# Performance work log

Hardware: AMD Instinct MI355X
Metric: run time of the kernel (lower is better)

The kernel has to match this reference:

```python
import jax, jax.numpy as jnp
import numpy as np
import math

D_MODEL = 1024
N_HEAD = 16
HEAD_DIM = D_MODEL // N_HEAD
SEQ_LEN = 512
INIT_SIZE = 1568  # from RelativeSinusoidalPositionalEmbedding default


def _rel_pos_embedding(seq_len, embedding_dim):
    # Replicates RelativeSinusoidalPositionalEmbedding with init_size=1568
    num_embeddings = INIT_SIZE + 1  # 1569
    half_dim = embedding_dim // 2
    scale = math.log(10000.0) / (half_dim - 1)
    freqs = np.exp(np.arange(half_dim, dtype=np.float32) * -scale)
    pos = np.arange(-(num_embeddings // 2), num_embeddings // 2, dtype=np.float32)  # [-785, 784)
    emb = pos[:, None] * freqs[None, :]
    weights = np.concatenate([np.sin(emb), np.cos(emb)], axis=1).astype(np.float32)  # (1569, d)
    weights[0, :] = 0.0  # padding_idx
    origin_shift = num_embeddings // 2 + 1  # 785
    positions = np.arange(-seq_len, seq_len) + origin_shift
    embed = weights[positions]  # (2*seq_len, d)
    return jnp.asarray(embed.T)  # (d, 2*seq_len), matching .T in __init__


def setup_inputs() -> dict:
    key = jax.random.key(0)
    k1, k2, k3, k4, k5 = jax.random.split(key, 5)
    x = jax.random.normal(k1, (8, SEQ_LEN, D_MODEL), dtype=jnp.float32)
    prev = jax.random.normal(k2, (8, N_HEAD, SEQ_LEN, SEQ_LEN), dtype=jnp.float32)
    # Linear(d_model, 3*d_model, bias=False): store as (d_model, 3*d_model) for x @ W
    Wqkv = jax.random.normal(k3, (D_MODEL, 3 * D_MODEL), dtype=jnp.float32) / math.sqrt(D_MODEL)
    r_r_bias = jax.random.normal(k4, (1, N_HEAD, 1, HEAD_DIM), dtype=jnp.float32) * 0.02
    r_w_bias = jax.random.normal(k5, (1, N_HEAD, 1, HEAD_DIM), dtype=jnp.float32) * 0.02
    rel_pos = _rel_pos_embedding(SEQ_LEN, HEAD_DIM)  # (head_dim, 2*seq_len)
    return {"x": x, "prev": prev, "Wqkv": Wqkv, "r_r_bias": r_r_bias,
            "r_w_bias": r_w_bias, "rel_pos": rel_pos, "skip_op": 1}


def _shift(BD, seq_len):
    # BD: (b, h, L, 2L) -> (b, h, L, L) via Transformer-XL pad/reshape trick
    b, h, L, two_L = BD.shape
    BD = jnp.pad(BD, ((0, 0), (0, 0), (0, 0), (0, 1)))        # (b,h,L,2L+1)
    BD = BD.reshape(b, h, -1, L)                               # (b,h,2L+1,L)
    BD = BD[:, :, :-1].reshape(b, h, L, -1)                    # (b,h,L,2L)
    return BD[:, :, :, seq_len:]                               # (b,h,L,L)


def reference(x, prev, Wqkv, r_r_bias, r_w_bias, rel_pos, skip_op):
    b, L, d = x.shape
    qkv = x @ Wqkv                                             # (b,L,3d)
    q, k, v = jnp.split(qkv, 3, axis=-1)
    q = q.reshape(b, L, N_HEAD, HEAD_DIM).transpose(0, 2, 1, 3)  # (b,h,L,hd)
    k = k.reshape(b, L, N_HEAD, HEAD_DIM).transpose(0, 2, 1, 3)
    v = v.reshape(b, L, N_HEAD, HEAD_DIM).transpose(0, 2, 1, 3)

    AC = jnp.einsum('bhqd,bhkd->bhqk', q + r_r_bias, k)
    BD = jnp.einsum('bhqd,dp->bhqp', q + r_w_bias, rel_pos)    # (b,h,L,2L)
    BD = _shift(BD, SEQ_LEN)
    E = jnp.einsum('bhkd,dp->bhkp', k, rel_pos)
    E = _shift(E, SEQ_LEN).transpose(0, 1, 3, 2)
    attn_score = (AC + BD + E) / math.sqrt(HEAD_DIM)
    if skip_op:
        attn_score = attn_score + prev
    prev_out = attn_score
    attn = jax.nn.softmax(attn_score, axis=-1)
    out = jnp.einsum('bhqk,bhkd->bhqd', attn, v)
    out = out.transpose(0, 2, 1, 3).reshape(b, L, d)
    return out, prev_out
```

## Files before the change

### kernel.cpp

```cpp
#include <hip/hip_runtime.h>
#include <hip/hip_bf16.h>
#include <math.h>

namespace {
constexpr int Bn = 8;
constexpr int Hn = 16;
constexpr int Ln = 512;
constexpr int HD = 64;
constexpr int DM = 1024;
constexpr int TL = 1024;
constexpr size_t QS  = (size_t)Bn * Hn * Ln * HD;
constexpr size_t FSz = (size_t)Hn * Ln * Ln;
constexpr size_t WN  = (size_t)DM * 3 * DM;
}

typedef __bf16 bf16x8 __attribute__((ext_vector_type(8)));
typedef float f32x4 __attribute__((ext_vector_type(4)));

typedef __attribute__((address_space(1))) void as1_void_t;
typedef __attribute__((address_space(3))) void as3_void_t;

__device__ __forceinline__ void gload_lds16(const void* g, void* l) {
  __builtin_amdgcn_global_load_lds((as1_void_t*)g, (as3_void_t*)l, 16, 0, 0);
}

__device__ __forceinline__ unsigned short f2bf(float f) {
  unsigned int u = __float_as_uint(f);
  u += 0x7fffu + ((u >> 16) & 1u);
  return (unsigned short)(u >> 16);
}
__device__ __forceinline__ float bf2f(unsigned short h) {
  return __uint_as_float(((unsigned int)h) << 16);
}

__global__ __launch_bounds__(256) void conv_x(const float* __restrict__ x,
                                              unsigned short* __restrict__ xh,
                                              unsigned short* __restrict__ xl) {
  size_t i = ((size_t)blockIdx.x * 256 + threadIdx.x) * 4;
  float4 v = *(const float4*)(x + i);
  unsigned short h0 = f2bf(v.x), h1 = f2bf(v.y), h2 = f2bf(v.z), h3 = f2bf(v.w);
  ushort4 hv = make_ushort4(h0, h1, h2, h3);
  ushort4 lv = make_ushort4(f2bf(v.x - bf2f(h0)), f2bf(v.y - bf2f(h1)),
                            f2bf(v.z - bf2f(h2)), f2bf(v.w - bf2f(h3)));
  *(ushort4*)(xh + i) = hv;
  *(ushort4*)(xl + i) = lv;
}

__global__ __launch_bounds__(256) void conv_w(const float* __restrict__ W,
                                              unsigned short* __restrict__ wh,
                                              unsigned short* __restrict__ wl) {
  __shared__ unsigned short Th[64][72];
  __shared__ unsigned short Tl[64][72];
  const int t = threadIdx.x;
  const int n0 = blockIdx.x * 64;
  const int k0 = blockIdx.y * 64;
#pragma unroll
  for (int i = 0; i < 4; ++i) {
    int row = i * 16 + (t >> 4);
    int col = (t & 15) * 4;
    float4 v = *(const float4*)(W + (size_t)(k0 + row) * 3072 + n0 + col);
    unsigned short h;
    h = f2bf(v.x); Th[row][col + 0] = h; Tl[row][col + 0] = f2bf(v.x - bf2f(h));
    h = f2bf(v.y); Th[row][col + 1] = h; Tl[row][col + 1] = f2bf(v.y - bf2f(h));
    h = f2bf(v.z); Th[row][col + 2] = h; Tl[row][col + 2] = f2bf(v.z - bf2f(h));
    h = f2bf(v.w); Th[row][col + 3] = h; Tl[row][col + 3] = f2bf(v.w - bf2f(h));
  }
  __syncthreads();
  const int rn = t & 63, qq = t >> 6;
  unsigned int hw[8], lw[8];
#pragma unroll
  for (int j = 0; j < 8; ++j) {
    unsigned short a = Th[qq * 16 + 2 * j][rn], b = Th[qq * 16 + 2 * j + 1][rn];
    hw[j] = (unsigned int)a | ((unsigned int)b << 16);
    unsigned short c = Tl[qq * 16 + 2 * j][rn], d = Tl[qq * 16 + 2 * j + 1][rn];
    lw[j] = (unsigned int)c | ((unsigned int)d << 16);
  }
  size_t o = (size_t)(n0 + rn) * 1024 + k0 + qq * 16;
  *(uint4*)(wh + o)     = make_uint4(hw[0], hw[1], hw[2], hw[3]);
  *(uint4*)(wh + o + 8) = make_uint4(hw[4], hw[5], hw[6], hw[7]);
  *(uint4*)(wl + o)     = make_uint4(lw[0], lw[1], lw[2], lw[3]);
  *(uint4*)(wl + o + 8) = make_uint4(lw[4], lw[5], lw[6], lw[7]);
}

__global__ __launch_bounds__(256, 2) void qkv_mfma(const unsigned short* __restrict__ xh,
                                                   const unsigned short* __restrict__ xl,
                                                   const unsigned short* __restrict__ wh,
                                                   const unsigned short* __restrict__ wl,
                                                   const float* __restrict__ rrb,
                                                   float* __restrict__ qarr,
                                                   float* __restrict__ karr,
                                                   unsigned short* __restrict__ qrh,
                                                   unsigned short* __restrict__ qrl,
                                                   unsigned short* __restrict__ kharr,
                                                   unsigned short* __restrict__ klarr,
                                                   unsigned short* __restrict__ vTh,
                                                   unsigned short* __restrict__ vTl) {
  __shared__ alignas(16) unsigned short Ah[128 * 32];
  __shared__ alignas(16) unsigned short Al[128 * 32];
  __shared__ alignas(16) unsigned short Bh[128 * 32];
  __shared__ alignas(16) unsigned short Bl[128 * 32];
  const int t = threadIdx.x;
  const int lane = t & 63;
  const int w = t >> 6;
  const int m0 = blockIdx.y * 128;
  const int n0 = blockIdx.x * 128;
  const int wr = w >> 1, wc = w & 1;
  const int l16 = lane & 15, s = lane >> 4;

  const unsigned short* gsrc = (w == 0) ? xh : (w == 1) ? xl : (w == 2) ? wh : wl;
  unsigned short* lbase = (w == 0) ? Ah : (w == 1) ? Al : (w == 2) ? Bh : Bl;
  const int rbase = (w < 2) ? m0 : n0;
  const int srow = lane >> 2, sc = lane & 3;

  int aoff[4], boff[4];
#pragma unroll
  for (int f = 0; f < 4; ++f) {
    int Rm = wr * 64 + f * 16 + l16;
    aoff[f] = Rm * 64 + ((s ^ ((Rm >> 1) & 3)) << 4);
    int Rn = wc * 64 + f * 16 + l16;
    boff[f] = Rn * 64 + ((s ^ ((Rn >> 1) & 3)) << 4);
  }

  f32x4 acc[4][4];
#pragma unroll
  for (int i = 0; i < 4; ++i)
#pragma unroll
    for (int j = 0; j < 4; ++j) acc[i][j] = (f32x4){0.f, 0.f, 0.f, 0.f};

  const char* Ahc = (const char*)Ah;
  const char* Alc = (const char*)Al;
  const char* Bhc = (const char*)Bh;
  const char* Blc = (const char*)Bl;

  for (int k0 = 0; k0 < 1024; k0 += 32) {
#pragma unroll
    for (int u = 0; u < 8; ++u) {
      int row = u * 16 + srow;
      int chunk = sc ^ ((row >> 1) & 3);
      gload_lds16(gsrc + (size_t)(rbase + row) * 1024 + k0 + chunk * 8,
                  lbase + u * 512);
    }
    __syncthreads();

    bf16x8 a_h[4], a_l[4], b_h[4], b_l[4];
#pragma unroll
    for (int f = 0; f < 4; ++f) {
      a_h[f] = *(const bf16x8*)(Ahc + aoff[f]);
      b_h[f] = *(const bf16x8*)(Bhc + boff[f]);
    }
#pragma unroll
    for (int i = 0; i < 4; ++i)
#pragma unroll
      for (int j = 0; j < 4; ++j)
        acc[i][j] = __builtin_amdgcn_mfma_f32_16x16x32_bf16(a_h[i], b_h[j], acc[i][j], 0, 0, 0);
#pragma unroll
    for (int f = 0; f < 4; ++f) b_l[f] = *(const bf16x8*)(Blc + boff[f]);
#pragma unroll
    for (int i = 0; i < 4; ++i)
#pragma unroll
      for (int j = 0; j < 4; ++j)
        acc[i][j] = __builtin_amdgcn_mfma_f32_16x16x32_bf16(a_h[i], b_l[j], acc[i][j], 0, 0, 0);
#pragma unroll
    for (int f = 0; f < 4; ++f) a_l[f] = *(const bf16x8*)(Alc + aoff[f]);
#pragma unroll
    for (int i = 0; i < 4; ++i)
#pragma unroll
      for (int j = 0; j < 4; ++j)
        acc[i][j] = __builtin_amdgcn_mfma_f32_16x16x32_bf16(a_l[i], b_h[j], acc[i][j], 0, 0, 0);
    __syncthreads();
  }

  const int part = n0 >> 10;
  const int nb = n0 & 1023;
#pragma unroll
  for (int i = 0; i < 4; ++i) {
#pragma unroll
    for (int j = 0; j < 4; ++j) {
      const int n = nb + wc * 64 + j * 16 + l16;
      const int h = n >> 6, d = n & 63;
      const int mb = m0 + wr * 64 + i * 16 + (lane >> 4) * 4;
      const int bb = mb >> 9, lb = mb & 511;
      const size_t rowbase = ((size_t)(bb * Hn + h) * Ln + lb) << 6;
      if (part == 0) {
        const float rr = rrb[h * HD + d];
#pragma unroll
        for (int r = 0; r < 4; ++r) {
          const float v = acc[i][j][r];
          const size_t qi = rowbase + ((size_t)r << 6) + d;
          qarr[qi] = v;
          const float qv = v + rr;
          const unsigned short hh = f2bf(qv);
          qrh[qi] = hh;
          qrl[qi] = f2bf(qv - bf2f(hh));
        }
      } else if (part == 1) {
#pragma unroll
        for (int r = 0; r < 4; ++r) {
          const float v = acc[i][j][r];
          const size_t qi = rowbase + ((size_t)r << 6) + d;
          karr[qi] = v;
          const unsigned short hh = f2bf(v);
          kharr[qi] = hh;
          klarr[qi] = f2bf(v - bf2f(hh));
        }
      } else {
        ushort4 hv, lv;
        unsigned short* hp = &hv.x;
        unsigned short* lp = &lv.x;
#pragma unroll
        for (int r = 0; r < 4; ++r) {
          const float v = acc[i][j][r];
          const unsigned short hh = f2bf(v);
          hp[r] = hh;
          lp[r] = f2bf(v - bf2f(hh));
        }
        const size_t vi = ((size_t)(bb * Hn + h) * HD + d) * Ln + lb;
        *(ushort4*)(vTh + vi) = hv;
        *(ushort4*)(vTl + vi) = lv;
      }
    }
  }
}

__global__ __launch_bounds__(256) void fg_gemm(const float* __restrict__ qarr,
                                               const float* __restrict__ karr,
                                               const float* __restrict__ rwb,
                                               const float* __restrict__ R,
                                               float* __restrict__ Fs,
                                               float* __restrict__ Gs,
                                               int b) {
  const int m0 = blockIdx.y * 64;
  const int n0 = blockIdx.x * 64;
  if (m0 + n0 + 126 < 512 || m0 + n0 >= 1024) return;

  __shared__ float As[64][68];
  __shared__ float Rs[64][68];
  const int t = threadIdx.x;
  const int h = blockIdx.z >> 1;
  const int which = blockIdx.z & 1;
  const float* A = (which == 0 ? qarr : karr) + (size_t)(b * Hn + h) * Ln * HD;

#pragma unroll
  for (int i = 0; i < 4; ++i) {
    int idx = t + i * 256;
    int r = idx >> 4;
    int c4 = (idx & 15) * 4;
    float4 av = *(const float4*)(A + (size_t)(m0 + r) * HD + c4);
    if (which == 0) {
      float4 bv = *(const float4*)(rwb + h * HD + c4);
      av.x += bv.x; av.y += bv.y; av.z += bv.z; av.w += bv.w;
    }
    As[c4 + 0][r] = av.x; As[c4 + 1][r] = av.y;
    As[c4 + 2][r] = av.z; As[c4 + 3][r] = av.w;
    *(float4*)(&Rs[r][c4]) = *(const float4*)(R + (size_t)r * TL + n0 + c4);
  }
  __syncthreads();
  const int tr = t >> 4, tc = t & 15;
  float acc[4][4];
#pragma unroll
  for (int i = 0; i < 4; ++i)
#pragma unroll
    for (int j = 0; j < 4; ++j) acc[i][j] = 0.f;
#pragma unroll 16
  for (int kk = 0; kk < 64; ++kk) {
    float a[4], bb[4];
    *(float4*)(a)  = *(const float4*)(&As[kk][tr * 4]);
    *(float4*)(bb) = *(const float4*)(&Rs[kk][tc * 4]);
#pragma unroll
    for (int i = 0; i < 4; ++i)
#pragma unroll
      for (int j = 0; j < 4; ++j) acc[i][j] = fmaf(a[i], bb[j], acc[i][j]);
  }
  if (which == 0) {
    float* O = Fs + (size_t)h * Ln * Ln;
#pragma unroll
    for (int i = 0; i < 4; ++i) {
      const int q = m0 + tr * 4 + i;
#pragma unroll
      for (int jj = 0; jj < 4; ++jj) {
        const int p = n0 + tc * 4 + jj;
        const int j = p + q - 512;
        if ((unsigned)j < 512u) O[((size_t)q << 9) + j] = acc[i][jj];
      }
    }
  } else {
    float* O = Gs + (size_t)h * Ln * Ln;
#pragma unroll
    for (int i = 0; i < 4; ++i) {
      const int jrow = m0 + tr * 4 + i;
#pragma unroll
      for (int jj = 0; jj < 4; ++jj) {
        const int p = n0 + tc * 4 + jj;
        const int q = p + jrow - 512;
        if ((unsigned)q < 512u) O[((size_t)q << 9) + jrow] = acc[i][jj];
      }
    }
  }
}

__global__ __launch_bounds__(64) void attn_mfma(const unsigned short* __restrict__ qrh,
                                                const unsigned short* __restrict__ qrl,
                                                const unsigned short* __restrict__ kharr,
                                                const unsigned short* __restrict__ klarr,
                                                const unsigned short* __restrict__ vTh,
                                                const unsigned short* __restrict__ vTl,
                                                const float* __restrict__ Fs,
                                                const float* __restrict__ Gs,
                                                const float* __restrict__ prev,
                                                const int* __restrict__ skip,
                                                float* __restrict__ out,
                                                float* __restrict__ pout,
                                                int b) {
  __shared__ alignas(16) unsigned short PhL[16 * 64];
  __shared__ alignas(16) unsigned short PlL[16 * 64];
  const int lane = threadIdx.x & 63;
  const int s = lane >> 4, l16 = lane & 15;
  const int h = blockIdx.y;
  const int q0 = blockIdx.x * 16;
  const size_t bh = (size_t)(b * Hn + h);
  const float pf = (skip[0] != 0) ? 1.f : 0.f;

  bf16x8 aqh[2], aql[2];
#pragma unroll
  for (int kd = 0; kd < 2; ++kd) {
    const size_t a = ((bh * Ln + q0 + l16) << 6) + kd * 32 + s * 8;
    aqh[kd] = *(const bf16x8*)(qrh + a);
    aql[kd] = *(const bf16x8*)(qrl + a);
  }

  float m_run[4] = {-INFINITY, -INFINITY, -INFINITY, -INFINITY};
  float l_run[4] = {0.f, 0.f, 0.f, 0.f};
  f32x4 O[4];
#pragma unroll
  for (int fo = 0; fo < 4; ++fo) O[fo] = (f32x4){0.f, 0.f, 0.f, 0.f};

  const int qrow = q0 + s * 4;

  for (int jt = 0; jt < 8; ++jt) {
    const int j0 = jt * 64;

    f32x4 S[4];
#pragma unroll
    for (int fi = 0; fi < 4; ++fi) S[fi] = (f32x4){0.f, 0.f, 0.f, 0.f};
#pragma unroll
    for (int kd = 0; kd < 2; ++kd) {
#pragma unroll
      for (int fi = 0; fi < 4; ++fi) {
        const size_t ka = ((bh * Ln + j0 + fi * 16 + l16) << 6) + kd * 32 + s * 8;
        const bf16x8 bkh = *(const bf16x8*)(kharr + ka);
        const bf16x8 bkl = *(const bf16x8*)(klarr + ka);
        S[fi] = __builtin_amdgcn_mfma_f32_16x16x32_bf16(aqh[kd], bkh, S[fi], 0, 0, 0);
        S[fi] = __builtin_amdgcn_mfma_f32_16x16x32_bf16(aqh[kd], bkl, S[fi], 0, 0, 0);
        S[fi] = __builtin_amdgcn_mfma_f32_16x16x32_bf16(aql[kd], bkh, S[fi], 0, 0, 0);
      }
    }

    float sc[4][4];
    float mx[4] = {-INFINITY, -INFINITY, -INFINITY, -INFINITY};
#pragma unroll
    for (int fi = 0; fi < 4; ++fi) {
      const int j = j0 + fi * 16 + l16;
#pragma unroll
      for (int r = 0; r < 4; ++r) {
        const int q = qrow + r;
        const size_t fb = (((size_t)h * Ln + q) << 9) + j;
        const size_t pb = ((bh * Ln + q) << 9) + j;
        const float v = (S[fi][r] + Fs[fb] + Gs[fb]) * 0.125f + pf * prev[pb];
        pout[pb] = v;
        sc[fi][r] = v;
        mx[r] = fmaxf(mx[r], v);
      }
    }

    float al[4];
#pragma unroll
    for (int r = 0; r < 4; ++r) {
      float m = mx[r];
      m = fmaxf(m, __shfl_xor(m, 1));
      m = fmaxf(m, __shfl_xor(m, 2));
      m = fmaxf(m, __shfl_xor(m, 4));
      m = fmaxf(m, __shfl_xor(m, 8));
      const float mn = fmaxf(m_run[r], m);
      al[r] = __expf(m_run[r] - mn);
      m_run[r] = mn;
    }

    float sum[4] = {0.f, 0.f, 0.f, 0.f};
#pragma unroll
    for (int fi = 0; fi < 4; ++fi) {
      const int jloc = fi * 16 + l16;
      const int chunk = jloc >> 3, sub = jloc & 7;
#pragma unroll
      for (int r = 0; r < 4; ++r) {
        const float p = __expf(sc[fi][r] - m_run[r]);
        sum[r] += p;
        const unsigned short ph = f2bf(p);
        const unsigned short pl = f2bf(p - bf2f(ph));
        const int qloc = s * 4 + r;
        const int idx = (qloc << 6) + ((chunk ^ (qloc & 7)) << 3) + sub;
        PhL[idx] = ph;
        PlL[idx] = pl;
      }
    }
#pragma unroll
    for (int r = 0; r < 4; ++r) {
      float sm = sum[r];
      sm += __shfl_xor(sm, 1);
      sm += __shfl_xor(sm, 2);
      sm += __shfl_xor(sm, 4);
      sm += __shfl_xor(sm, 8);
      l_run[r] = l_run[r] * al[r] + sm;
    }

#pragma unroll
    for (int fo = 0; fo < 4; ++fo)
#pragma unroll
      for (int r = 0; r < 4; ++r) O[fo][r] *= al[r];

#pragma unroll
    for (int kj = 0; kj < 2; ++kj) {
      const int raddr = (l16 << 6) + (((kj * 4 + s) ^ (l16 & 7)) << 3);
      const bf16x8 pah = *(const bf16x8*)(PhL + raddr);
      const bf16x8 pal = *(const bf16x8*)(PlL + raddr);
#pragma unroll
      for (int fo = 0; fo < 4; ++fo) {
        const size_t va = ((bh << 6) + fo * 16 + l16) * (size_t)Ln + j0 + kj * 32 + s * 8;
        const bf16x8 vbh = *(const bf16x8*)(vTh + va);
        const bf16x8 vbl = *(const bf16x8*)(vTl + va);
        O[fo] = __builtin_amdgcn_mfma_f32_16x16x32_bf16(pah, vbh, O[fo], 0, 0, 0);
        O[fo] = __builtin_amdgcn_mfma_f32_16x16x32_bf16(pah, vbl, O[fo], 0, 0, 0);
        O[fo] = __builtin_amdgcn_mfma_f32_16x16x32_bf16(pal, vbh, O[fo], 0, 0, 0);
      }
    }
  }

#pragma unroll
  for (int r = 0; r < 4; ++r) {
    const float inv = 1.0f / l_run[r];
    const size_t ob = ((size_t)b * Ln + qrow + r) * DM + h * HD;
#pragma unroll
    for (int fo = 0; fo < 4; ++fo) {
      out[ob + fo * 16 + l16] = O[fo][r] * inv;
    }
  }
}

extern "C" void kernel_launch(void* const* d_in, const int* in_sizes, int n_in,
                              void* d_out, int out_size, void* d_ws, size_t ws_size,
                              hipStream_t stream) {
  const float* x    = (const float*)d_in[0];
  const float* prev = (const float*)d_in[1];
  const float* W    = (const float*)d_in[2];
  const float* rrb  = (const float*)d_in[3];
  const float* rwb  = (const float*)d_in[4];
  const float* R    = (const float*)d_in[5];
  const int*   skip = (const int*)d_in[6];

  float* out  = (float*)d_out;
  float* pout = out + (size_t)Bn * Ln * DM;

  float* ws = (float*)d_ws;
  float* qarr = ws;
  float* karr = ws + QS;
  unsigned short* qrh = (unsigned short*)(ws + 2 * QS);
  unsigned short* qrl = qrh + QS;
  unsigned short* kh  = qrl + QS;
  unsigned short* kl  = kh + QS;
  unsigned short* vTh = kl + QS;
  unsigned short* vTl = vTh + QS;
  float* Farr = ws + 5 * QS;
  float* Garr = Farr + FSz;

  unsigned short* xh = (unsigned short*)Farr;
  unsigned short* xl = xh + QS;
  unsigned short* wwh = xl + QS;
  unsigned short* wwl = wwh + WN;

  conv_x<<<dim3(4096), 256, 0, stream>>>(x, xh, xl);
  conv_w<<<dim3(48, 16), 256, 0, stream>>>(W, wwh, wwl);
  qkv_mfma<<<dim3(24, 32), 256, 0, stream>>>(xh, xl, wwh, wwl, rrb, qarr, karr,
                                             qrh, qrl, kh, kl, vTh, vTl);
  for (int b = 0; b < Bn; ++b) {
    fg_gemm<<<dim3(TL / 64, Ln / 64, Hn * 2), 256, 0, stream>>>(qarr, karr, rwb, R, Farr, Garr, b);
    attn_mfma<<<dim3(Ln / 16, Hn), 64, 0, stream>>>(qrh, qrl, kh, kl, vTh, vTl,
                                                    Farr, Garr, prev, skip, out, pout, b);
  }
}
```

Measured before the change: 1.118 ms.

## Split attention key loop across four waves and drop fp32 Q/K stores

The attention kernel now runs four wavefronts per block. Each wave covers two of the eight 64-key tiles and keeps its own online-softmax state, and the partial outputs are merged through shared memory with a max/sum rescale. This gives each 16-query tile more parallelism and shortens the serial key loop. Separately, the QKV GEMM stops writing fp32 copies of Q and K. The positional GEMM rebuilds them from the bf16 hi/lo split, adding rw-rr bias correction to Q, which cuts global write and read traffic. The cost is shared-memory reduction overhead, extra synchronisation, and slight precision loss from the hi+lo reconstruction.

```diff
diff --git a/kernel.cpp b/kernel.cpp
--- a/kernel.cpp
+++ b/kernel.cpp
@@ -87,8 +87,6 @@
                                                    const unsigned short* __restrict__ wh,
                                                    const unsigned short* __restrict__ wl,
                                                    const float* __restrict__ rrb,
-                                                   float* __restrict__ qarr,
-                                                   float* __restrict__ karr,
                                                    unsigned short* __restrict__ qrh,
                                                    unsigned short* __restrict__ qrl,
                                                    unsigned short* __restrict__ kharr,
@@ -185,10 +183,8 @@
         const float rr = rrb[h * HD + d];
 #pragma unroll
         for (int r = 0; r < 4; ++r) {
-          const float v = acc[i][j][r];
+          const float qv = acc[i][j][r] + rr;
           const size_t qi = rowbase + ((size_t)r << 6) + d;
-          qarr[qi] = v;
-          const float qv = v + rr;
           const unsigned short hh = f2bf(qv);
           qrh[qi] = hh;
           qrl[qi] = f2bf(qv - bf2f(hh));
@@ -198,7 +194,6 @@
         for (int r = 0; r < 4; ++r) {
           const float v = acc[i][j][r];
           const size_t qi = rowbase + ((size_t)r << 6) + d;
-          karr[qi] = v;
           const unsigned short hh = f2bf(v);
           kharr[qi] = hh;
           klarr[qi] = f2bf(v - bf2f(hh));
@@ -222,8 +217,11 @@
   }
 }
 
-__global__ __launch_bounds__(256) void fg_gemm(const float* __restrict__ qarr,
-                                               const float* __restrict__ karr,
+__global__ __launch_bounds__(256) void fg_gemm(const unsigned short* __restrict__ qrh,
+                                               const unsigned short* __restrict__ qrl,
+                                               const unsigned short* __restrict__ kharr,
+                                               const unsigned short* __restrict__ klarr,
+                                               const float* __restrict__ rrb,
                                                const float* __restrict__ rwb,
                                                const float* __restrict__ R,
                                                float* __restrict__ Fs,
@@ -238,20 +236,29 @@
   const int t = threadIdx.x;
   const int h = blockIdx.z >> 1;
   const int which = blockIdx.z & 1;
-  const float* A = (which == 0 ? qarr : karr) + (size_t)(b * Hn + h) * Ln * HD;
+  const size_t abase = (size_t)(b * Hn + h) * Ln * HD;
+  const unsigned short* Ahp = (which == 0 ? qrh : kharr) + abase;
+  const unsigned short* Alp = (which == 0 ? qrl : klarr) + abase;
 
 #pragma unroll
   for (int i = 0; i < 4; ++i) {
     int idx = t + i * 256;
     int r = idx >> 4;
     int c4 = (idx & 15) * 4;
-    float4 av = *(const float4*)(A + (size_t)(m0 + r) * HD + c4);
+    ushort4 h4 = *(const ushort4*)(Ahp + (size_t)(m0 + r) * HD + c4);
+    ushort4 l4 = *(const ushort4*)(Alp + (size_t)(m0 + r) * HD + c4);
+    float vx = bf2f(h4.x) + bf2f(l4.x);
+    float vy = bf2f(h4.y) + bf2f(l4.y);
+    float vz = bf2f(h4.z) + bf2f(l4.z);
+    float vw = bf2f(h4.w) + bf2f(l4.w);
     if (which == 0) {
-      float4 bv = *(const float4*)(rwb + h * HD + c4);
-      av.x += bv.x; av.y += bv.y; av.z += bv.z; av.w += bv.w;
-    }
-    As[c4 + 0][r] = av.x; As[c4 + 1][r] = av.y;
-    As[c4 + 2][r] = av.z; As[c4 + 3][r] = av.w;
+      float4 rr = *(const float4*)(rrb + h * HD + c4);
+      float4 rw = *(const float4*)(rwb + h * HD + c4);
+      vx += rw.x - rr.x; vy += rw.y - rr.y;
+      vz += rw.z - rr.z; vw += rw.w - rr.w;
+    }
+    As[c4 + 0][r] = vx; As[c4 + 1][r] = vy;
+    As[c4 + 2][r] = vz; As[c4 + 3][r] = vw;
     *(float4*)(&Rs[r][c4]) = *(const float4*)(R + (size_t)r * TL + n0 + c4);
   }
   __syncthreads();
@@ -298,22 +305,28 @@
   }
 }
 
-__global__ __launch_bounds__(64) void attn_mfma(const unsigned short* __restrict__ qrh,
-                                                const unsigned short* __restrict__ qrl,
-                                                const unsigned short* __restrict__ kharr,
-                                                const unsigned short* __restrict__ klarr,
-                                                const unsigned short* __restrict__ vTh,
-                                                const unsigned short* __restrict__ vTl,
-                                                const float* __restrict__ Fs,
-                                                const float* __restrict__ Gs,
-                                                const float* __restrict__ prev,
-                                                const int* __restrict__ skip,
-                                                float* __restrict__ out,
-                                                float* __restrict__ pout,
-                                                int b) {
-  __shared__ alignas(16) unsigned short PhL[16 * 64];
-  __shared__ alignas(16) unsigned short PlL[16 * 64];
-  const int lane = threadIdx.x & 63;
+__global__ __launch_bounds__(256) void attn_mfma(const unsigned short* __restrict__ qrh,
+                                                 const unsigned short* __restrict__ qrl,
+                                                 const unsigned short* __restrict__ kharr,
+                                                 const unsigned short* __restrict__ klarr,
+                                                 const unsigned short* __restrict__ vTh,
+                                                 const unsigned short* __restrict__ vTl,
+                                                 const float* __restrict__ Fs,
+                                                 const float* __restrict__ Gs,
+                                                 const float* __restrict__ prev,
+                                                 const int* __restrict__ skip,
+                                                 float* __restrict__ out,
+                                                 float* __restrict__ pout,
+                                                 int b) {
+  __shared__ alignas(16) unsigned short PhL[4][16 * 64];
+  __shared__ alignas(16) unsigned short PlL[4][16 * 64];
+  __shared__ float Om[4][16][65];
+  __shared__ float mw[4][16];
+  __shared__ float lw[4][16];
+
+  const int t = threadIdx.x;
+  const int w = t >> 6;
+  const int lane = t & 63;
   const int s = lane >> 4, l16 = lane & 15;
   const int h = blockIdx.y;
   const int q0 = blockIdx.x * 16;
@@ -335,9 +348,12 @@
   for (int fo = 0; fo < 4; ++fo) O[fo] = (f32x4){0.f, 0.f, 0.f, 0.f};
 
   const int qrow = q0 + s * 4;
-
-  for (int jt = 0; jt < 8; ++jt) {
-    const int j0 = jt * 64;
+  unsigned short* PhW = &PhL[w][0];
+  unsigned short* PlW = &PlL[w][0];
+
+#pragma unroll
+  for (int it = 0; it < 2; ++it) {
+    const int j0 = (w * 2 + it) * 64;
 
     f32x4 S[4];
 #pragma unroll
@@ -398,8 +414,8 @@
         const unsigned short pl = f2bf(p - bf2f(ph));
         const int qloc = s * 4 + r;
         const int idx = (qloc << 6) + ((chunk ^ (qloc & 7)) << 3) + sub;
-        PhL[idx] = ph;
-        PlL[idx] = pl;
+        PhW[idx] = ph;
+        PlW[idx] = pl;
       }
     }
 #pragma unroll
@@ -420,8 +436,8 @@
 #pragma unroll
     for (int kj = 0; kj < 2; ++kj) {
       const int raddr = (l16 << 6) + (((kj * 4 + s) ^ (l16 & 7)) << 3);
-      const bf16x8 pah = *(const bf16x8*)(PhL + raddr);
-      const bf16x8 pal = *(const bf16x8*)(PlL + raddr);
+      const bf16x8 pah = *(const bf16x8*)(PhW + raddr);
+      const bf16x8 pal = *(const bf16x8*)(PlW + raddr);
 #pragma unroll
       for (int fo = 0; fo < 4; ++fo) {
         const size_t va = ((bh << 6) + fo * 16 + l16) * (size_t)Ln + j0 + kj * 32 + s * 8;
@@ -434,14 +450,42 @@
     }
   }
 
+  if (l16 == 0) {
+#pragma unroll
+    for (int r = 0; r < 4; ++r) {
+      mw[w][s * 4 + r] = m_run[r];
+      lw[w][s * 4 + r] = l_run[r];
+    }
+  }
+  __syncthreads();
+
+  float fw[4];
 #pragma unroll
   for (int r = 0; r < 4; ++r) {
-    const float inv = 1.0f / l_run[r];
-    const size_t ob = ((size_t)b * Ln + qrow + r) * DM + h * HD;
-#pragma unroll
-    for (int fo = 0; fo < 4; ++fo) {
-      out[ob + fo * 16 + l16] = O[fo][r] * inv;
-    }
+    const int ql_ = s * 4 + r;
+    const float g = fmaxf(fmaxf(mw[0][ql_], mw[1][ql_]), fmaxf(mw[2][ql_], mw[3][ql_]));
+    fw[r] = __expf(m_run[r] - g);
+  }
+#pragma unroll
+  for (int fo = 0; fo < 4; ++fo)
+#pragma unroll
+    for (int r = 0; r < 4; ++r)
+      Om[w][s * 4 + r][fo * 16 + l16] = O[fo][r] * fw[r];
+  __syncthreads();
+
+  {
+    const int q = t >> 4;
+    const int d0 = (t & 15) * 4;
+    const float g = fmaxf(fmaxf(mw[0][q], mw[1][q]), fmaxf(mw[2][q], mw[3][q]));
+    const float lt = lw[0][q] * __expf(mw[0][q] - g) + lw[1][q] * __expf(mw[1][q] - g) +
+                     lw[2][q] * __expf(mw[2][q] - g) + lw[3][q] * __expf(mw[3][q] - g);
+    const float inv = 1.0f / lt;
+    float4 o4;
+    o4.x = (Om[0][q][d0 + 0] + Om[1][q][d0 + 0] + Om[2][q][d0 + 0] + Om[3][q][d0 + 0]) * inv;
+    o4.y = (Om[0][q][d0 + 1] + Om[1][q][d0 + 1] + Om[2][q][d0 + 1] + Om[3][q][d0 + 1]) * inv;
+    o4.z = (Om[0][q][d0 + 2] + Om[1][q][d0 + 2] + Om[2][q][d0 + 2] + Om[3][q][d0 + 2]) * inv;
+    o4.w = (Om[0][q][d0 + 3] + Om[1][q][d0 + 3] + Om[2][q][d0 + 3] + Om[3][q][d0 + 3]) * inv;
+    *(float4*)(out + ((size_t)b * Ln + q0 + q) * DM + h * HD + d0) = o4;
   }
 }
 
@@ -460,15 +504,13 @@
   float* pout = out + (size_t)Bn * Ln * DM;
 
   float* ws = (float*)d_ws;
-  float* qarr = ws;
-  float* karr = ws + QS;
-  unsigned short* qrh = (unsigned short*)(ws + 2 * QS);
+  unsigned short* qrh = (unsigned short*)ws;
   unsigned short* qrl = qrh + QS;
   unsigned short* kh  = qrl + QS;
   unsigned short* kl  = kh + QS;
   unsigned short* vTh = kl + QS;
   unsigned short* vTl = vTh + QS;
-  float* Farr = ws + 5 * QS;
+  float* Farr = ws + 3 * QS;
   float* Garr = Farr + FSz;
 
   unsigned short* xh = (unsigned short*)Farr;
@@ -478,11 +520,12 @@
 
   conv_x<<<dim3(4096), 256, 0, stream>>>(x, xh, xl);
   conv_w<<<dim3(48, 16), 256, 0, stream>>>(W, wwh, wwl);
-  qkv_mfma<<<dim3(24, 32), 256, 0, stream>>>(xh, xl, wwh, wwl, rrb, qarr, karr,
+  qkv_mfma<<<dim3(24, 32), 256, 0, stream>>>(xh, xl, wwh, wwl, rrb,
                                              qrh, qrl, kh, kl, vTh, vTl);
   for (int b = 0; b < Bn; ++b) {
-    fg_gemm<<<dim3(TL / 64, Ln / 64, Hn * 2), 256, 0, stream>>>(qarr, karr, rwb, R, Farr, Garr, b);
-    attn_mfma<<<dim3(Ln / 16, Hn), 64, 0, stream>>>(qrh, qrl, kh, kl, vTh, vTl,
-                                                    Farr, Garr, prev, skip, out, pout, b);
-  }
-}
+    fg_gemm<<<dim3(TL / 64, Ln / 64, Hn * 2), 256, 0, stream>>>(qrh, qrl, kh, kl, rrb, rwb, R,
+                                                                Farr, Garr, b);
+    attn_mfma<<<dim3(Ln / 16, Hn), 256, 0, stream>>>(qrh, qrl, kh, kl, vTh, vTl,
+                                                     Farr, Garr, prev, skip, out, pout, b);
+  }
+}
```

Measured after the change: 977.5 us. -12.6%, faster.
